# Kernel tuning notes

Measured on AMD Instinct MI355X. Metric: run time of the kernel, lower is better.

Reference implementation:

```python
import jax, jax.numpy as jnp
import numpy as np

IN_SIZE = 256
HID = 256          # memory_vector_size == hidd_size
MEM = 128          # memory_size
ALPHA_SIG = -0.4
GAMMA = 0.3
GATE = 1.0 / (1.0 + np.exp(-ALPHA_SIG))  # sigmoid(alpha_sig) ~ 0.4013
B, T = 128, 1024


def _l2norm(x):
    # F.normalize(x, dim=-1): x / max(||x||2, 1e-12)
    return x / jnp.maximum(jnp.linalg.norm(x, axis=-1, keepdims=True), 1e-12)


def setup_inputs() -> dict:
    key = jax.random.key(0)
    ks = jax.random.split(key, 5)
    s = 1.0 / np.sqrt(HID)  # torch LSTMCell default init range
    X = jax.random.normal(ks[0], (B, T, IN_SIZE), dtype=jnp.float32)
    W_ih = jax.random.uniform(ks[1], (4 * HID, IN_SIZE), jnp.float32, -s, s)
    W_hh = jax.random.uniform(ks[2], (4 * HID, HID), jnp.float32, -s, s)
    b_ih = jax.random.uniform(ks[3], (4 * HID,), jnp.float32, -s, s)
    b_hh = jax.random.uniform(ks[4], (4 * HID,), jnp.float32, -s, s)
    return {"X": X, "W_ih": W_ih, "W_hh": W_hh, "b_ih": b_ih, "b_hh": b_hh}


def _forward(X, W_ih, W_hh, b_ih, b_hh):
    Bt = X.shape[0]
    gate = jnp.asarray(GATE, X.dtype)
    gamma = jnp.asarray(GAMMA, X.dtype)

    def lstm_cell(x, h, c):
        z = x @ W_ih.T + b_ih + h @ W_hh.T + b_hh  # [B, 4H]
        i, f, g, o = jnp.split(z, 4, axis=-1)
        c_new = jax.nn.sigmoid(f) * c + jax.nn.sigmoid(i) * jnp.tanh(g)
        h_new = jax.nn.sigmoid(o) * jnp.tanh(c_new)
        return h_new, c_new

    def step(carry, x_t):
        h, c, M, w_u, prev_w_r = carry
        h, c = lstm_cell(x_t, h, c)
        # read head: softmax over cosine similarity with memory rows
        inner = h @ M.T                                    # [B, MEM]
        denom = (jnp.linalg.norm(h, axis=-1, keepdims=True)
                 * jnp.linalg.norm(M, axis=-1)[None, :])   # [B, MEM]
        w_r = jax.nn.softmax(inner / (denom + 1e-8), axis=-1)
        read = w_r @ M                                     # [B, H]
        out_t = jnp.concatenate([h, read], axis=-1)        # [B, 2H]
        # write (original is under torch.no_grad / detached)
        hs = jax.lax.stop_gradient(h)
        wrs = jax.lax.stop_gradient(w_r)
        w_lu = (1.0 - gate) * jax.nn.one_hot(jnp.argmin(w_u, axis=-1), MEM, dtype=M.dtype)
        w_w = gate * prev_w_r + w_lu                       # [B, MEM]
        M_new = _l2norm(M + w_w.T @ hs)                    # einsum('bi,bj->bij').sum(0) == w_w.T @ h
        w_u_new = _l2norm(gamma * w_u + wrs + w_w)
        return (h, c, M_new, w_u_new, wrs), out_t

    init = (jnp.zeros((Bt, HID), X.dtype),
            jnp.zeros((Bt, HID), X.dtype),
            jnp.zeros((MEM, HID), X.dtype),   # self.M starts as zeros
            jnp.zeros((Bt, MEM), X.dtype),    # w_u
            jnp.zeros((Bt, MEM), X.dtype))    # prev_w_r
    _, ys = jax.lax.scan(step, init, jnp.swapaxes(X, 0, 1))  # ys: [T, B, 2H]
    return jnp.swapaxes(ys, 0, 1)                            # [B, T, 2H]


def reference(X, W_ih, W_hh, b_ih, b_hh):
    return _forward(X, W_ih, W_hh, b_ih, b_hh)
```

## Files before the change

### kernel.cpp

```cpp
#include <hip/hip_runtime.h>
#include <math.h>

#define BATCH 128
#define TSTEPS 1024
#define INSZ 256
#define HSZ 256
#define MEMN 128

#define NWG_A 128
#define NWG_B 64
#define NWG_C 32
#define NWG 224
#define NTHR 256

#define GATE_C 0.40131233988754794f
#define OMG_C  (1.0f - GATE_C)
#define GAMMA_C 0.3f

__device__ float g_hT[(size_t)TSTEPS * HSZ * BATCH];
__device__ float g_M [(size_t)TSTEPS * MEMN * HSZ];
__device__ float g_Mn[(size_t)TSTEPS * MEMN];
__device__ float g_ww[(size_t)TSTEPS * BATCH * MEMN];
__device__ float g_c[BATCH * HSZ];
__device__ int g_fA[TSTEPS * NWG_A];
__device__ int g_fB[TSTEPS * NWG_B];
__device__ int g_fC[TSTEPS * NWG_C];

__global__ void reset_ctrl_kernel() {
    const int gt = blockIdx.x * 256 + threadIdx.x, gn = gridDim.x * 256;
    for (int i = gt; i < TSTEPS * NWG_A; i += gn)
        __hip_atomic_store(&g_fA[i], 0, __ATOMIC_RELAXED, __HIP_MEMORY_SCOPE_AGENT);
    for (int i = gt; i < TSTEPS * NWG_B; i += gn)
        __hip_atomic_store(&g_fB[i], 0, __ATOMIC_RELAXED, __HIP_MEMORY_SCOPE_AGENT);
    for (int i = gt; i < TSTEPS * NWG_C; i += gn)
        __hip_atomic_store(&g_fC[i], 0, __ATOMIC_RELAXED, __HIP_MEMORY_SCOPE_AGENT);
}

__device__ __forceinline__ float sigf(float x) { return 1.0f / (1.0f + expf(-x)); }

__device__ __forceinline__ void st_wt(float* p, float v) {
    __hip_atomic_store(p, v, __ATOMIC_RELAXED, __HIP_MEMORY_SCOPE_AGENT);
}
__device__ __forceinline__ void st_flag(int* p, int v) {
    __hip_atomic_store(p, v, __ATOMIC_RELAXED, __HIP_MEMORY_SCOPE_AGENT);
}
__device__ __forceinline__ void wait_vm0() { asm volatile("s_waitcnt vmcnt(0)" ::: "memory"); }

__device__ __forceinline__ void wait_flags(int* f, int n, int want, int lane) {
    int it = 0;
    for (;;) {
        bool ok = true;
        for (int i = lane; i < n; i += 64)
            ok &= (__hip_atomic_load(&f[i], __ATOMIC_RELAXED, __HIP_MEMORY_SCOPE_AGENT) == want);
        if (__all(ok)) break;
        __builtin_amdgcn_s_sleep(1);
        if (++it > (1 << 22)) break;
    }
}

__global__ void __launch_bounds__(NTHR, 1)
mann_persist(const float* __restrict__ X, const float* __restrict__ Wih,
             const float* __restrict__ Whh, const float* __restrict__ bih,
             const float* __restrict__ bhh, float* __restrict__ out) {
    __shared__ float4 s_x4[64 * 128];
    __shared__ float s_aux[4096];
    __shared__ float s_red8[8];
    __shared__ float s_red16[16];
    __shared__ unsigned long long s_redu8[8];

    const int w = blockIdx.x, tid = threadIdx.x;
    const int lane = tid & 63, wv = tid >> 6;

    auto grpsum = [&](float v) -> float {
#pragma unroll
        for (int o = 32; o; o >>= 1) v += __shfl_xor(v, o, 64);
        if (lane == 0) s_red8[wv] = v;
        __syncthreads();
        float r = s_red8[(tid >> 7) * 2] + s_red8[(tid >> 7) * 2 + 1];
        __syncthreads();
        return r;
    };
    auto grpmax = [&](float v) -> float {
#pragma unroll
        for (int o = 32; o; o >>= 1) v = fmaxf(v, __shfl_xor(v, o, 64));
        if (lane == 0) s_red8[wv] = v;
        __syncthreads();
        float r = fmaxf(s_red8[(tid >> 7) * 2], s_red8[(tid >> 7) * 2 + 1]);
        __syncthreads();
        return r;
    };
    auto grpminu = [&](unsigned long long v) -> unsigned long long {
#pragma unroll
        for (int o = 32; o; o >>= 1) {
            unsigned long long o2 = __shfl_xor(v, o, 64);
            v = (o2 < v) ? o2 : v;
        }
        if (lane == 0) s_redu8[wv] = v;
        __syncthreads();
        unsigned long long a = s_redu8[(tid >> 7) * 2], b2 = s_redu8[(tid >> 7) * 2 + 1];
        unsigned long long r = (a < b2) ? a : b2;
        __syncthreads();
        return r;
    };
    auto red256sum4 = [&](float v0, float v1, float v2, float v3, float (&r)[4]) {
#pragma unroll
        for (int o = 32; o; o >>= 1) {
            v0 += __shfl_xor(v0, o, 64);
            v1 += __shfl_xor(v1, o, 64);
            v2 += __shfl_xor(v2, o, 64);
            v3 += __shfl_xor(v3, o, 64);
        }
        if (lane == 0) {
            s_red16[wv * 4 + 0] = v0; s_red16[wv * 4 + 1] = v1;
            s_red16[wv * 4 + 2] = v2; s_red16[wv * 4 + 3] = v3;
        }
        __syncthreads();
#pragma unroll
        for (int k = 0; k < 4; ++k)
            r[k] = (s_red16[0 * 4 + k] + s_red16[1 * 4 + k]) +
                   (s_red16[2 * 4 + k] + s_red16[3 * 4 + k]);
        __syncthreads();
    };

    if (w < NWG_A) {
        const int bb = w >> 6, jb = w & 63;
        const int bglob = bb * 64 + lane;
        float biasA[4];
#pragma unroll
        for (int g = 0; g < 4; ++g) {
            const int row = g * HSZ + jb * 4 + wv;
            biasA[g] = bih[row] + bhh[row];
        }

        auto stageX = [&](int t) {
            const int kq = tid & 63, bofs = tid >> 6;
#pragma unroll 4
            for (int rep = 0; rep < 16; ++rep) {
                const int b = rep * 4 + bofs;
                const float4 v = *(const float4*)(X + ((size_t)(bb * 64 + b) * TSTEPS + t) * INSZ + kq * 4);
                s_x4[b * 128 + (kq ^ (b & 7))] = v;
            }
        };
        auto computeRegion = [&](float (&acc)[16], const float* __restrict__ Wb, const int kofs) {
            const int kbase = kofs + wv * 64;
#pragma unroll 4
            for (int k4 = 0; k4 < 16; ++k4) {
                const int kg = kbase + k4 * 4;
                const float4 xv = s_x4[lane * 128 + ((kg >> 2) ^ (lane & 7))];
                const int kl = kg - kofs;
#pragma unroll
                for (int rr = 0; rr < 16; ++rr) {
                    const int grow = (rr >> 2) * HSZ + jb * 4 + (rr & 3);
                    const float4 wv4 = *(const float4*)(Wb + (size_t)grow * 256 + kl);
                    acc[rr] += wv4.x * xv.x + wv4.y * xv.y + wv4.z * xv.z + wv4.w * xv.w;
                }
            }
        };

        stageX(0);
        __syncthreads();

        for (int t = 0; t < TSTEPS; ++t) {
            float acc[16];
#pragma unroll
            for (int i = 0; i < 16; ++i) acc[i] = 0.f;
            float4 hv[16];
            if (t > 0) {
                if (wv == 0) wait_flags(g_fA + (size_t)(t - 1) * NWG_A, NWG_A, t, lane);
                __syncthreads();
                asm volatile("" ::: "memory");
#pragma unroll
                for (int rep = 0; rep < 16; ++rep) {
                    const int j0 = (wv * 16 + rep) * 4;
                    const size_t base = ((size_t)(t - 1) * HSZ + j0) * BATCH + bglob;
                    float4 v;
                    v.x = g_hT[base];
                    v.y = g_hT[base + BATCH];
                    v.z = g_hT[base + 2 * BATCH];
                    v.w = g_hT[base + 3 * BATCH];
                    hv[rep] = v;
                }
            }
            computeRegion(acc, Wih, 0);
            if (t > 0) {
#pragma unroll
                for (int rep = 0; rep < 16; ++rep)
                    s_x4[lane * 128 + ((64 + wv * 16 + rep) ^ (lane & 7))] = hv[rep];
            } else {
                const float4 z4 = make_float4(0.f, 0.f, 0.f, 0.f);
#pragma unroll
                for (int rep = 0; rep < 16; ++rep)
                    s_x4[lane * 128 + ((64 + wv * 16 + rep) ^ (lane & 7))] = z4;
            }
            __syncthreads();
            computeRegion(acc, Whh, 256);
#pragma unroll
            for (int rr = 0; rr < 16; ++rr) s_aux[(wv * 16 + rr) * 64 + lane] = acc[rr];
            __syncthreads();
            float z[4];
#pragma unroll
            for (int g = 0; g < 4; ++g) {
                const int rr = g * 4 + wv;
                z[g] = ((s_aux[rr * 64 + lane] + s_aux[(16 + rr) * 64 + lane]) +
                        (s_aux[(32 + rr) * 64 + lane] + s_aux[(48 + rr) * 64 + lane])) + biasA[g];
            }
            const int jglob = jb * 4 + wv;
            const int cidx = bglob * HSZ + jglob;
            const float cold = (t == 0) ? 0.f : g_c[cidx];
            const float cn = sigf(z[1]) * cold + sigf(z[0]) * tanhf(z[2]);
            const float hn = sigf(z[3]) * tanhf(cn);
            g_c[cidx] = cn;
            st_wt(&g_hT[((size_t)t * HSZ + jglob) * BATCH + bglob], hn);
            wait_vm0();
            __syncthreads();
            if (tid == 0) st_flag(&g_fA[(size_t)t * NWG_A + w], t + 1);
            if (t + 1 < TSTEPS) stageX(t + 1);
        }
    } else if (w < NWG_A + NWG_B) {
        const int bwg = w - NWG_A;
        const int grp = tid >> 7, lm = tid & 127;
        const int bB = bwg * 2 + grp;
        float* s_M = (float*)s_x4;
        float* s_h2 = s_aux;
        float* s_wr2 = s_aux + 512;
        float wwreg = (lm == 0) ? OMG_C : 0.f;
        float wureg = 0.f;

        for (int t = 0; t < TSTEPS; ++t) {
            if (t > 0) {
                if (wv == 1) wait_flags(g_fC + (size_t)(t - 1) * NWG_C, NWG_C, t, lane);
                __syncthreads();
                asm volatile("" ::: "memory");
                float4 mt[32];
                const float4* msrc = (const float4*)&g_M[(size_t)t * MEMN * HSZ];
#pragma unroll
                for (int i = 0; i < 32; ++i) mt[i] = msrc[i * 256 + tid];
                float4* md = (float4*)s_M;
#pragma unroll
                for (int i = 0; i < 32; ++i) md[i * 256 + tid] = mt[i];
            }
            if (wv == 0) wait_flags(g_fA + (size_t)t * NWG_A, NWG_A, t + 1, lane);
            __syncthreads();
            asm volatile("" ::: "memory");
            s_h2[grp * 256 + lm] = g_hT[((size_t)t * HSZ + lm) * BATCH + bB];
            s_h2[grp * 256 + lm + 128] = g_hT[((size_t)t * HSZ + lm + 128) * BATCH + bB];
            __syncthreads();
            const float hv0 = s_h2[grp * 256 + lm], hv1 = s_h2[grp * 256 + lm + 128];
            const float hnorm = sqrtf(grpsum(hv0 * hv0 + hv1 * hv1));
            float sc = 0.f;
            if (t > 0) {
                const float4* mrow = (const float4*)&s_M[(size_t)lm * HSZ];
                const float4* h4 = (const float4*)&s_h2[grp * 256];
                const int sw = lm & 7;
                float a = 0.f;
#pragma unroll 8
                for (int c = 0; c < 64; ++c) {
                    const int ci = c ^ sw;
                    const float4 m4 = mrow[ci], x4 = h4[ci];
                    a += m4.x * x4.x + m4.y * x4.y + m4.z * x4.z + m4.w * x4.w;
                }
                const float mn = g_Mn[(size_t)t * MEMN + lm];
                sc = a / (hnorm * mn + 1e-8f);
            }
            const float mx = grpmax(sc);
            const float ev = expf(sc - mx);
            const float es = grpsum(ev);
            const float wr = ev / es;
            s_wr2[grp * 128 + lm] = wr;
            __syncthreads();
            float rd0 = 0.f, rd1 = 0.f;
            if (t > 0) {
#pragma unroll 8
                for (int m = 0; m < 128; ++m) {
                    const float mv = s_M[m * HSZ + tid];
                    rd0 += s_wr2[m] * mv;
                    rd1 += s_wr2[128 + m] * mv;
                }
            }
            const int b0 = bwg * 2, b1 = b0 + 1;
            float* o0 = out + ((size_t)b0 * TSTEPS + t) * 512;
            float* o1 = out + ((size_t)b1 * TSTEPS + t) * 512;
            o0[tid] = s_h2[tid];
            o1[tid] = s_h2[256 + tid];
            o0[256 + tid] = rd0;
            o1[256 + tid] = rd1;
            const float un = GAMMA_C * wureg + wr + wwreg;
            const float un2 = grpsum(un * un);
            const float us = 1.0f / fmaxf(sqrtf(un2), 1e-12f);
            const float wun = un * us;
            wureg = wun;
            unsigned long long key =
                (((unsigned long long)__float_as_uint(wun)) << 32) | (unsigned)lm;
            const unsigned long long mk = grpminu(key);
            const int amin = (int)(mk & 0xffffffffu);
            const float wwn = GATE_C * wr + ((lm == amin) ? OMG_C : 0.f);
            wwreg = wwn;
            if (t + 1 < TSTEPS)
                st_wt(&g_ww[((size_t)(t + 1) * BATCH + bB) * MEMN + lm], wwn);
            wait_vm0();
            __syncthreads();
            if (tid == 0) st_flag(&g_fB[(size_t)t * NWG_B + bwg], t + 1);
        }
    } else {
        const int cwg = w - NWG_A - NWG_B;
        const int m0 = cwg * 4;
        float* s_wwc = s_aux;
        float mreg[4] = {0.f, 0.f, 0.f, 0.f};

        for (int t = 0; t < TSTEPS - 1; ++t) {
            if (wv == 1 && t > 0) wait_flags(g_fB + (size_t)(t - 1) * NWG_B, NWG_B, t, lane);
            __syncthreads();
            asm volatile("" ::: "memory");
            {
                const int e0 = tid, e1 = tid + 256;
                float v0, v1;
                if (t > 0) {
                    v0 = g_ww[((size_t)t * BATCH + (e0 >> 2)) * MEMN + m0 + (e0 & 3)];
                    v1 = g_ww[((size_t)t * BATCH + (e1 >> 2)) * MEMN + m0 + (e1 & 3)];
                } else {
                    v0 = (m0 + (e0 & 3) == 0) ? OMG_C : 0.f;
                    v1 = (m0 + (e1 & 3) == 0) ? OMG_C : 0.f;
                }
                s_wwc[(e0 & 3) * 128 + (e0 >> 2)] = v0;
                s_wwc[(e1 & 3) * 128 + (e1 >> 2)] = v1;
            }
            if (wv == 0) wait_flags(g_fA + (size_t)t * NWG_A, NWG_A, t + 1, lane);
            __syncthreads();
            asm volatile("" ::: "memory");
            float4 hb[32];
            const float4* ht4 = (const float4*)&g_hT[((size_t)t * HSZ + tid) * BATCH];
#pragma unroll
            for (int q = 0; q < 32; ++q) hb[q] = ht4[q];
            float macc[4];
#pragma unroll
            for (int mi = 0; mi < 4; ++mi) macc[mi] = mreg[mi];
#pragma unroll
            for (int b4 = 0; b4 < 32; ++b4) {
                const float4 hv4 = hb[b4];
#pragma unroll
                for (int mi = 0; mi < 4; ++mi) {
                    const float* wc = &s_wwc[mi * 128 + b4 * 4];
                    macc[mi] += wc[0] * hv4.x + wc[1] * hv4.y + wc[2] * hv4.z + wc[3] * hv4.w;
                }
            }
            float nr[4];
            red256sum4(macc[0] * macc[0], macc[1] * macc[1],
                       macc[2] * macc[2], macc[3] * macc[3], nr);
#pragma unroll
            for (int mi = 0; mi < 4; ++mi) {
                const float nrm = sqrtf(nr[mi]);
                const float scale = 1.0f / fmaxf(nrm, 1e-12f);
                const float vo = macc[mi] * scale;
                mreg[mi] = vo;
                st_wt(&g_M[((size_t)(t + 1) * MEMN + m0 + mi) * HSZ + tid], vo);
                if (tid == 0) st_wt(&g_Mn[(size_t)(t + 1) * MEMN + m0 + mi], nrm * scale);
            }
            wait_vm0();
            __syncthreads();
            if (tid == 0) st_flag(&g_fC[(size_t)t * NWG_C + cwg], t + 1);
        }
    }
}

extern "C" void kernel_launch(void* const* d_in, const int* in_sizes, int n_in,
                              void* d_out, int out_size, void* d_ws, size_t ws_size,
                              hipStream_t stream) {
    const float* X   = (const float*)d_in[0];
    const float* Wih = (const float*)d_in[1];
    const float* Whh = (const float*)d_in[2];
    const float* bih = (const float*)d_in[3];
    const float* bhh = (const float*)d_in[4];
    float* out = (float*)d_out;
    (void)in_sizes; (void)n_in; (void)out_size; (void)d_ws; (void)ws_size;

    hipLaunchKernelGGL(reset_ctrl_kernel, dim3(224), dim3(256), 0, stream);
    hipLaunchKernelGGL(mann_persist, dim3(NWG), dim3(NTHR), 0, stream,
                       X, Wih, Whh, bih, bhh, out);
}
```

Before: 24.68 ms.

## Interleave workgroup roles across grid, prefetch X into registers, keep cell state in registers

Workgroup roles are now assigned by blockIdx modulo 8, which interleaves LSTM, read-head and memory-write groups across the device. The grid grows to 256 and class 7 sits idle. The next timestep's X slice is loaded into registers before the W_ih product and the flag wait, so its global latency overlaps compute. The flag wait is split across the four waves, and the LSTM cell state c stays in a register instead of a round trip through global memory. In exchange, register pressure rises from the 16 prefetched float4 values, and 32 extra idle workgroups are launched.

After: 23.69 ms. 1.04x faster.

```diff
diff --git a/kernel.cpp b/kernel.cpp
--- a/kernel.cpp
+++ b/kernel.cpp
@@ -10,7 +10,7 @@
 #define NWG_A 128
 #define NWG_B 64
 #define NWG_C 32
-#define NWG 224
+#define NWG 256
 #define NTHR 256
 
 #define GATE_C 0.40131233988754794f
@@ -21,7 +21,6 @@
 __device__ float g_M [(size_t)TSTEPS * MEMN * HSZ];
 __device__ float g_Mn[(size_t)TSTEPS * MEMN];
 __device__ float g_ww[(size_t)TSTEPS * BATCH * MEMN];
-__device__ float g_c[BATCH * HSZ];
 __device__ int g_fA[TSTEPS * NWG_A];
 __device__ int g_fB[TSTEPS * NWG_B];
 __device__ int g_fC[TSTEPS * NWG_C];
@@ -70,6 +69,7 @@
 
     const int w = blockIdx.x, tid = threadIdx.x;
     const int lane = tid & 63, wv = tid >> 6;
+    const int cls = w & 7, idx8 = w >> 3;
 
     auto grpsum = [&](float v) -> float {
 #pragma unroll
@@ -122,8 +122,10 @@
         __syncthreads();
     };
 
-    if (w < NWG_A) {
-        const int bb = w >> 6, jb = w & 63;
+    if (cls < 4) {
+        const int aidx = cls * 32 + idx8;
+        const int bb = cls >> 1;
+        const int jb = (cls & 1) * 32 + idx8;
         const int bglob = bb * 64 + lane;
         float biasA[4];
 #pragma unroll
@@ -132,13 +134,20 @@
             biasA[g] = bih[row] + bhh[row];
         }
 
-        auto stageX = [&](int t) {
+        auto loadXreg = [&](int t, float4 (&xr)[16]) {
             const int kq = tid & 63, bofs = tid >> 6;
-#pragma unroll 4
+#pragma unroll
             for (int rep = 0; rep < 16; ++rep) {
                 const int b = rep * 4 + bofs;
-                const float4 v = *(const float4*)(X + ((size_t)(bb * 64 + b) * TSTEPS + t) * INSZ + kq * 4);
-                s_x4[b * 128 + (kq ^ (b & 7))] = v;
+                xr[rep] = *(const float4*)(X + ((size_t)(bb * 64 + b) * TSTEPS + t) * INSZ + kq * 4);
+            }
+        };
+        auto storeXlds = [&](float4 (&xr)[16]) {
+            const int kq = tid & 63, bofs = tid >> 6;
+#pragma unroll
+            for (int rep = 0; rep < 16; ++rep) {
+                const int b = rep * 4 + bofs;
+                s_x4[b * 128 + (kq ^ (b & 7))] = xr[rep];
             }
         };
         auto computeRegion = [&](float (&acc)[16], const float* __restrict__ Wb, const int kofs) {
@@ -157,18 +166,27 @@
             }
         };
 
-        stageX(0);
-        __syncthreads();
+        {
+            float4 xr[16];
+            loadXreg(0, xr);
+            storeXlds(xr);
+        }
+        __syncthreads();
+        float creg = 0.f;
 
         for (int t = 0; t < TSTEPS; ++t) {
             float acc[16];
 #pragma unroll
             for (int i = 0; i < 16; ++i) acc[i] = 0.f;
-            float4 hv[16];
+            const bool pf = (t + 1 < TSTEPS);
+            float4 xr[16];
+            if (pf) loadXreg(t + 1, xr);
+            computeRegion(acc, Wih, 0);
             if (t > 0) {
-                if (wv == 0) wait_flags(g_fA + (size_t)(t - 1) * NWG_A, NWG_A, t, lane);
+                wait_flags(g_fA + (size_t)(t - 1) * NWG_A + wv * 32, 32, t, lane);
                 __syncthreads();
                 asm volatile("" ::: "memory");
+                float4 hv[16];
 #pragma unroll
                 for (int rep = 0; rep < 16; ++rep) {
                     const int j0 = (wv * 16 + rep) * 4;
@@ -180,13 +198,13 @@
                     v.w = g_hT[base + 3 * BATCH];
                     hv[rep] = v;
                 }
-            }
-            computeRegion(acc, Wih, 0);
-            if (t > 0) {
+                if (pf) storeXlds(xr);
 #pragma unroll
                 for (int rep = 0; rep < 16; ++rep)
                     s_x4[lane * 128 + ((64 + wv * 16 + rep) ^ (lane & 7))] = hv[rep];
             } else {
+                __syncthreads();
+                if (pf) storeXlds(xr);
                 const float4 z4 = make_float4(0.f, 0.f, 0.f, 0.f);
 #pragma unroll
                 for (int rep = 0; rep < 16; ++rep)
@@ -205,19 +223,16 @@
                         (s_aux[(32 + rr) * 64 + lane] + s_aux[(48 + rr) * 64 + lane])) + biasA[g];
             }
             const int jglob = jb * 4 + wv;
-            const int cidx = bglob * HSZ + jglob;
-            const float cold = (t == 0) ? 0.f : g_c[cidx];
-            const float cn = sigf(z[1]) * cold + sigf(z[0]) * tanhf(z[2]);
+            const float cn = sigf(z[1]) * creg + sigf(z[0]) * tanhf(z[2]);
             const float hn = sigf(z[3]) * tanhf(cn);
-            g_c[cidx] = cn;
+            creg = cn;
             st_wt(&g_hT[((size_t)t * HSZ + jglob) * BATCH + bglob], hn);
             wait_vm0();
             __syncthreads();
-            if (tid == 0) st_flag(&g_fA[(size_t)t * NWG_A + w], t + 1);
-            if (t + 1 < TSTEPS) stageX(t + 1);
-        }
-    } else if (w < NWG_A + NWG_B) {
-        const int bwg = w - NWG_A;
+            if (tid == 0) st_flag(&g_fA[(size_t)t * NWG_A + aidx], t + 1);
+        }
+    } else if (cls < 6) {
+        const int bwg = (cls - 4) * 32 + idx8;
         const int grp = tid >> 7, lm = tid & 127;
         const int bB = bwg * 2 + grp;
         float* s_M = (float*)s_x4;
@@ -301,8 +316,8 @@
             __syncthreads();
             if (tid == 0) st_flag(&g_fB[(size_t)t * NWG_B + bwg], t + 1);
         }
-    } else {
-        const int cwg = w - NWG_A - NWG_B;
+    } else if (cls == 6) {
+        const int cwg = idx8;
         const int m0 = cwg * 4;
         float* s_wwc = s_aux;
         float mreg[4] = {0.f, 0.f, 0.f, 0.f};
```

## Replace persistent flag-synchronised kernel with per-timestep kernel launches

Applied to the files above, without the earlier changes.

Replaces the single persistent kernel, which coordinated LSTM, read-head and memory-write workgroups through spin-waited global flags, with one launch per timestep. Kernel boundaries now provide ordering, and the read/write stages are skewed one step behind the LSTM stage. Recurrent state such as w_u and w_w that used to stay in registers now goes through global memory. The change removes flag polling and cross-workgroup spinning but adds about a thousand launches and their overheads. It also loses the previous overlap of X staging with the wait for the next step.

Measured after the change: 24.56 ms. No clear change (-0.5%).

```diff
diff --git a/kernel.cpp b/kernel.cpp
--- a/kernel.cpp
+++ b/kernel.cpp
@@ -17,51 +17,20 @@
 #define OMG_C  (1.0f - GATE_C)
 #define GAMMA_C 0.3f
 
-__device__ float g_hT[(size_t)TSTEPS * HSZ * BATCH];
-__device__ float g_M [(size_t)TSTEPS * MEMN * HSZ];
-__device__ float g_Mn[(size_t)TSTEPS * MEMN];
-__device__ float g_ww[(size_t)TSTEPS * BATCH * MEMN];
-__device__ float g_c[BATCH * HSZ];
-__device__ int g_fA[TSTEPS * NWG_A];
-__device__ int g_fB[TSTEPS * NWG_B];
-__device__ int g_fC[TSTEPS * NWG_C];
-
-__global__ void reset_ctrl_kernel() {
-    const int gt = blockIdx.x * 256 + threadIdx.x, gn = gridDim.x * 256;
-    for (int i = gt; i < TSTEPS * NWG_A; i += gn)
-        __hip_atomic_store(&g_fA[i], 0, __ATOMIC_RELAXED, __HIP_MEMORY_SCOPE_AGENT);
-    for (int i = gt; i < TSTEPS * NWG_B; i += gn)
-        __hip_atomic_store(&g_fB[i], 0, __ATOMIC_RELAXED, __HIP_MEMORY_SCOPE_AGENT);
-    for (int i = gt; i < TSTEPS * NWG_C; i += gn)
-        __hip_atomic_store(&g_fC[i], 0, __ATOMIC_RELAXED, __HIP_MEMORY_SCOPE_AGENT);
-}
+__device__ float g_hT [(size_t)TSTEPS * HSZ * BATCH];
+__device__ float g_M  [(size_t)TSTEPS * MEMN * HSZ];
+__device__ float g_Mn [(size_t)TSTEPS * MEMN];
+__device__ float g_ww [(size_t)(TSTEPS + 1) * BATCH * MEMN];
+__device__ float g_wu [(size_t)(TSTEPS + 1) * BATCH * MEMN];
+__device__ float g_cst[BATCH * HSZ];
 
 __device__ __forceinline__ float sigf(float x) { return 1.0f / (1.0f + expf(-x)); }
 
-__device__ __forceinline__ void st_wt(float* p, float v) {
-    __hip_atomic_store(p, v, __ATOMIC_RELAXED, __HIP_MEMORY_SCOPE_AGENT);
-}
-__device__ __forceinline__ void st_flag(int* p, int v) {
-    __hip_atomic_store(p, v, __ATOMIC_RELAXED, __HIP_MEMORY_SCOPE_AGENT);
-}
-__device__ __forceinline__ void wait_vm0() { asm volatile("s_waitcnt vmcnt(0)" ::: "memory"); }
-
-__device__ __forceinline__ void wait_flags(int* f, int n, int want, int lane) {
-    int it = 0;
-    for (;;) {
-        bool ok = true;
-        for (int i = lane; i < n; i += 64)
-            ok &= (__hip_atomic_load(&f[i], __ATOMIC_RELAXED, __HIP_MEMORY_SCOPE_AGENT) == want);
-        if (__all(ok)) break;
-        __builtin_amdgcn_s_sleep(1);
-        if (++it > (1 << 22)) break;
-    }
-}
-
 __global__ void __launch_bounds__(NTHR, 1)
-mann_persist(const float* __restrict__ X, const float* __restrict__ Wih,
-             const float* __restrict__ Whh, const float* __restrict__ bih,
-             const float* __restrict__ bhh, float* __restrict__ out) {
+step_kernel(const int t,
+            const float* __restrict__ X, const float* __restrict__ Wih,
+            const float* __restrict__ Whh, const float* __restrict__ bih,
+            const float* __restrict__ bhh, float* __restrict__ out) {
     __shared__ float4 s_x4[64 * 128];
     __shared__ float s_aux[4096];
     __shared__ float s_red8[8];
@@ -123,16 +92,20 @@
     };
 
     if (w < NWG_A) {
+        if (t >= TSTEPS) return;
         const int bb = w >> 6, jb = w & 63;
         const int bglob = bb * 64 + lane;
+        const int jglob = jb * 4 + wv;
+        const int cidx = bglob * HSZ + jglob;
         float biasA[4];
 #pragma unroll
         for (int g = 0; g < 4; ++g) {
             const int row = g * HSZ + jb * 4 + wv;
             biasA[g] = bih[row] + bhh[row];
         }
-
-        auto stageX = [&](int t) {
+        const float cold = (t == 0) ? 0.f : g_cst[cidx];
+
+        {
             const int kq = tid & 63, bofs = tid >> 6;
 #pragma unroll 4
             for (int rep = 0; rep < 16; ++rep) {
@@ -140,8 +113,31 @@
                 const float4 v = *(const float4*)(X + ((size_t)(bb * 64 + b) * TSTEPS + t) * INSZ + kq * 4);
                 s_x4[b * 128 + (kq ^ (b & 7))] = v;
             }
-        };
-        auto computeRegion = [&](float (&acc)[16], const float* __restrict__ Wb, const int kofs) {
+        }
+        float4 hv[16];
+        if (t > 0) {
+#pragma unroll
+            for (int rep = 0; rep < 16; ++rep) {
+                const int j0 = (wv * 16 + rep) * 4;
+                const size_t base = ((size_t)(t - 1) * HSZ + j0) * BATCH + bglob;
+                float4 v;
+                v.x = g_hT[base];
+                v.y = g_hT[base + BATCH];
+                v.z = g_hT[base + 2 * BATCH];
+                v.w = g_hT[base + 3 * BATCH];
+                hv[rep] = v;
+            }
+        } else {
+            const float4 z4 = make_float4(0.f, 0.f, 0.f, 0.f);
+#pragma unroll
+            for (int rep = 0; rep < 16; ++rep) hv[rep] = z4;
+        }
+        __syncthreads();
+
+        float acc[16];
+#pragma unroll
+        for (int i = 0; i < 16; ++i) acc[i] = 0.f;
+        auto computeRegion = [&](float (&a16)[16], const float* __restrict__ Wb, const int kofs) {
             const int kbase = kofs + wv * 64;
 #pragma unroll 4
             for (int k4 = 0; k4 < 16; ++k4) {
@@ -152,212 +148,152 @@
                 for (int rr = 0; rr < 16; ++rr) {
                     const int grow = (rr >> 2) * HSZ + jb * 4 + (rr & 3);
                     const float4 wv4 = *(const float4*)(Wb + (size_t)grow * 256 + kl);
-                    acc[rr] += wv4.x * xv.x + wv4.y * xv.y + wv4.z * xv.z + wv4.w * xv.w;
+                    a16[rr] += wv4.x * xv.x + wv4.y * xv.y + wv4.z * xv.z + wv4.w * xv.w;
                 }
             }
         };
-
-        stageX(0);
-        __syncthreads();
-
-        for (int t = 0; t < TSTEPS; ++t) {
-            float acc[16];
-#pragma unroll
-            for (int i = 0; i < 16; ++i) acc[i] = 0.f;
-            float4 hv[16];
-            if (t > 0) {
-                if (wv == 0) wait_flags(g_fA + (size_t)(t - 1) * NWG_A, NWG_A, t, lane);
-                __syncthreads();
-                asm volatile("" ::: "memory");
-#pragma unroll
-                for (int rep = 0; rep < 16; ++rep) {
-                    const int j0 = (wv * 16 + rep) * 4;
-                    const size_t base = ((size_t)(t - 1) * HSZ + j0) * BATCH + bglob;
-                    float4 v;
-                    v.x = g_hT[base];
-                    v.y = g_hT[base + BATCH];
-                    v.z = g_hT[base + 2 * BATCH];
-                    v.w = g_hT[base + 3 * BATCH];
-                    hv[rep] = v;
-                }
-            }
-            computeRegion(acc, Wih, 0);
-            if (t > 0) {
-#pragma unroll
-                for (int rep = 0; rep < 16; ++rep)
-                    s_x4[lane * 128 + ((64 + wv * 16 + rep) ^ (lane & 7))] = hv[rep];
-            } else {
-                const float4 z4 = make_float4(0.f, 0.f, 0.f, 0.f);
-#pragma unroll
-                for (int rep = 0; rep < 16; ++rep)
-                    s_x4[lane * 128 + ((64 + wv * 16 + rep) ^ (lane & 7))] = z4;
-            }
-            __syncthreads();
-            computeRegion(acc, Whh, 256);
-#pragma unroll
-            for (int rr = 0; rr < 16; ++rr) s_aux[(wv * 16 + rr) * 64 + lane] = acc[rr];
-            __syncthreads();
-            float z[4];
-#pragma unroll
-            for (int g = 0; g < 4; ++g) {
-                const int rr = g * 4 + wv;
-                z[g] = ((s_aux[rr * 64 + lane] + s_aux[(16 + rr) * 64 + lane]) +
-                        (s_aux[(32 + rr) * 64 + lane] + s_aux[(48 + rr) * 64 + lane])) + biasA[g];
-            }
-            const int jglob = jb * 4 + wv;
-            const int cidx = bglob * HSZ + jglob;
-            const float cold = (t == 0) ? 0.f : g_c[cidx];
-            const float cn = sigf(z[1]) * cold + sigf(z[0]) * tanhf(z[2]);
-            const float hn = sigf(z[3]) * tanhf(cn);
-            g_c[cidx] = cn;
-            st_wt(&g_hT[((size_t)t * HSZ + jglob) * BATCH + bglob], hn);
-            wait_vm0();
-            __syncthreads();
-            if (tid == 0) st_flag(&g_fA[(size_t)t * NWG_A + w], t + 1);
-            if (t + 1 < TSTEPS) stageX(t + 1);
-        }
+        computeRegion(acc, Wih, 0);
+#pragma unroll
+        for (int rep = 0; rep < 16; ++rep)
+            s_x4[lane * 128 + ((64 + wv * 16 + rep) ^ (lane & 7))] = hv[rep];
+        __syncthreads();
+        computeRegion(acc, Whh, 256);
+#pragma unroll
+        for (int rr = 0; rr < 16; ++rr) s_aux[(wv * 16 + rr) * 64 + lane] = acc[rr];
+        __syncthreads();
+        float z[4];
+#pragma unroll
+        for (int g = 0; g < 4; ++g) {
+            const int rr = g * 4 + wv;
+            z[g] = ((s_aux[rr * 64 + lane] + s_aux[(16 + rr) * 64 + lane]) +
+                    (s_aux[(32 + rr) * 64 + lane] + s_aux[(48 + rr) * 64 + lane])) + biasA[g];
+        }
+        const float cn = sigf(z[1]) * cold + sigf(z[0]) * tanhf(z[2]);
+        const float hn = sigf(z[3]) * tanhf(cn);
+        g_cst[cidx] = cn;
+        g_hT[((size_t)t * HSZ + jglob) * BATCH + bglob] = hn;
     } else if (w < NWG_A + NWG_B) {
+        if (t < 1) return;
+        const int s = t - 1;
         const int bwg = w - NWG_A;
         const int grp = tid >> 7, lm = tid & 127;
         const int bB = bwg * 2 + grp;
         float* s_M = (float*)s_x4;
         float* s_h2 = s_aux;
         float* s_wr2 = s_aux + 512;
-        float wwreg = (lm == 0) ? OMG_C : 0.f;
-        float wureg = 0.f;
-
-        for (int t = 0; t < TSTEPS; ++t) {
-            if (t > 0) {
-                if (wv == 1) wait_flags(g_fC + (size_t)(t - 1) * NWG_C, NWG_C, t, lane);
-                __syncthreads();
-                asm volatile("" ::: "memory");
-                float4 mt[32];
-                const float4* msrc = (const float4*)&g_M[(size_t)t * MEMN * HSZ];
-#pragma unroll
-                for (int i = 0; i < 32; ++i) mt[i] = msrc[i * 256 + tid];
-                float4* md = (float4*)s_M;
-#pragma unroll
-                for (int i = 0; i < 32; ++i) md[i * 256 + tid] = mt[i];
-            }
-            if (wv == 0) wait_flags(g_fA + (size_t)t * NWG_A, NWG_A, t + 1, lane);
-            __syncthreads();
-            asm volatile("" ::: "memory");
-            s_h2[grp * 256 + lm] = g_hT[((size_t)t * HSZ + lm) * BATCH + bB];
-            s_h2[grp * 256 + lm + 128] = g_hT[((size_t)t * HSZ + lm + 128) * BATCH + bB];
-            __syncthreads();
-            const float hv0 = s_h2[grp * 256 + lm], hv1 = s_h2[grp * 256 + lm + 128];
-            const float hnorm = sqrtf(grpsum(hv0 * hv0 + hv1 * hv1));
-            float sc = 0.f;
-            if (t > 0) {
-                const float4* mrow = (const float4*)&s_M[(size_t)lm * HSZ];
-                const float4* h4 = (const float4*)&s_h2[grp * 256];
-                const int sw = lm & 7;
-                float a = 0.f;
+
+        if (s > 0) {
+            float4 mt[32];
+            const float4* msrc = (const float4*)&g_M[(size_t)s * MEMN * HSZ];
+#pragma unroll
+            for (int i = 0; i < 32; ++i) mt[i] = msrc[i * 256 + tid];
+            float4* md = (float4*)s_M;
+#pragma unroll
+            for (int i = 0; i < 32; ++i) md[i * 256 + tid] = mt[i];
+        }
+        s_h2[grp * 256 + lm] = g_hT[((size_t)s * HSZ + lm) * BATCH + bB];
+        s_h2[grp * 256 + lm + 128] = g_hT[((size_t)s * HSZ + lm + 128) * BATCH + bB];
+        const float wu_prev = (s > 0) ? g_wu[((size_t)s * BATCH + bB) * MEMN + lm] : 0.f;
+        const float ww_prev = (s > 0) ? g_ww[((size_t)s * BATCH + bB) * MEMN + lm]
+                                      : ((lm == 0) ? OMG_C : 0.f);
+        __syncthreads();
+        const float hv0 = s_h2[grp * 256 + lm], hv1 = s_h2[grp * 256 + lm + 128];
+        const float hnorm = sqrtf(grpsum(hv0 * hv0 + hv1 * hv1));
+        float sc = 0.f;
+        if (s > 0) {
+            const float4* mrow = (const float4*)&s_M[(size_t)lm * HSZ];
+            const float4* h4 = (const float4*)&s_h2[grp * 256];
+            const int sw = lm & 7;
+            float a = 0.f;
 #pragma unroll 8
-                for (int c = 0; c < 64; ++c) {
-                    const int ci = c ^ sw;
-                    const float4 m4 = mrow[ci], x4 = h4[ci];
-                    a += m4.x * x4.x + m4.y * x4.y + m4.z * x4.z + m4.w * x4.w;
-                }
-                const float mn = g_Mn[(size_t)t * MEMN + lm];
-                sc = a / (hnorm * mn + 1e-8f);
-            }
-            const float mx = grpmax(sc);
-            const float ev = expf(sc - mx);
-            const float es = grpsum(ev);
-            const float wr = ev / es;
-            s_wr2[grp * 128 + lm] = wr;
-            __syncthreads();
-            float rd0 = 0.f, rd1 = 0.f;
-            if (t > 0) {
+            for (int c = 0; c < 64; ++c) {
+                const int ci = c ^ sw;
+                const float4 m4 = mrow[ci], x4 = h4[ci];
+                a += m4.x * x4.x + m4.y * x4.y + m4.z * x4.z + m4.w * x4.w;
+            }
+            const float mn = g_Mn[(size_t)s * MEMN + lm];
+            sc = a / (hnorm * mn + 1e-8f);
+        }
+        const float mx = grpmax(sc);
+        const float ev = expf(sc - mx);
+        const float es = grpsum(ev);
+        const float wr = ev / es;
+        s_wr2[grp * 128 + lm] = wr;
+        __syncthreads();
+        float rd0 = 0.f, rd1 = 0.f;
+        if (s > 0) {
 #pragma unroll 8
-                for (int m = 0; m < 128; ++m) {
-                    const float mv = s_M[m * HSZ + tid];
-                    rd0 += s_wr2[m] * mv;
-                    rd1 += s_wr2[128 + m] * mv;
-                }
-            }
-            const int b0 = bwg * 2, b1 = b0 + 1;
-            float* o0 = out + ((size_t)b0 * TSTEPS + t) * 512;
-            float* o1 = out + ((size_t)b1 * TSTEPS + t) * 512;
-            o0[tid] = s_h2[tid];
-            o1[tid] = s_h2[256 + tid];
-            o0[256 + tid] = rd0;
-            o1[256 + tid] = rd1;
-            const float un = GAMMA_C * wureg + wr + wwreg;
-            const float un2 = grpsum(un * un);
-            const float us = 1.0f / fmaxf(sqrtf(un2), 1e-12f);
-            const float wun = un * us;
-            wureg = wun;
-            unsigned long long key =
-                (((unsigned long long)__float_as_uint(wun)) << 32) | (unsigned)lm;
-            const unsigned long long mk = grpminu(key);
-            const int amin = (int)(mk & 0xffffffffu);
-            const float wwn = GATE_C * wr + ((lm == amin) ? OMG_C : 0.f);
-            wwreg = wwn;
-            if (t + 1 < TSTEPS)
-                st_wt(&g_ww[((size_t)(t + 1) * BATCH + bB) * MEMN + lm], wwn);
-            wait_vm0();
-            __syncthreads();
-            if (tid == 0) st_flag(&g_fB[(size_t)t * NWG_B + bwg], t + 1);
-        }
-    } else {
+            for (int m = 0; m < 128; ++m) {
+                const float mv = s_M[m * HSZ + tid];
+                rd0 += s_wr2[m] * mv;
+                rd1 += s_wr2[128 + m] * mv;
+            }
+        }
+        const int b0 = bwg * 2, b1 = b0 + 1;
+        float* o0 = out + ((size_t)b0 * TSTEPS + s) * 512;
+        float* o1 = out + ((size_t)b1 * TSTEPS + s) * 512;
+        o0[tid] = s_h2[tid];
+        o1[tid] = s_h2[256 + tid];
+        o0[256 + tid] = rd0;
+        o1[256 + tid] = rd1;
+        const float un = GAMMA_C * wu_prev + wr + ww_prev;
+        const float un2 = grpsum(un * un);
+        const float us = 1.0f / fmaxf(sqrtf(un2), 1e-12f);
+        const float wun = un * us;
+        g_wu[((size_t)(s + 1) * BATCH + bB) * MEMN + lm] = wun;
+        unsigned long long key =
+            (((unsigned long long)__float_as_uint(wun)) << 32) | (unsigned)lm;
+        const unsigned long long mk = grpminu(key);
+        const int amin = (int)(mk & 0xffffffffu);
+        const float wwn = GATE_C * wr + ((lm == amin) ? OMG_C : 0.f);
+        g_ww[((size_t)(s + 1) * BATCH + bB) * MEMN + lm] = wwn;
+    } else if (w < NWG) {
+        if (t < 1 || t - 1 >= TSTEPS - 1) return;
+        const int s = t - 1;
         const int cwg = w - NWG_A - NWG_B;
         const int m0 = cwg * 4;
         float* s_wwc = s_aux;
-        float mreg[4] = {0.f, 0.f, 0.f, 0.f};
-
-        for (int t = 0; t < TSTEPS - 1; ++t) {
-            if (wv == 1 && t > 0) wait_flags(g_fB + (size_t)(t - 1) * NWG_B, NWG_B, t, lane);
-            __syncthreads();
-            asm volatile("" ::: "memory");
-            {
-                const int e0 = tid, e1 = tid + 256;
-                float v0, v1;
-                if (t > 0) {
-                    v0 = g_ww[((size_t)t * BATCH + (e0 >> 2)) * MEMN + m0 + (e0 & 3)];
-                    v1 = g_ww[((size_t)t * BATCH + (e1 >> 2)) * MEMN + m0 + (e1 & 3)];
-                } else {
-                    v0 = (m0 + (e0 & 3) == 0) ? OMG_C : 0.f;
-                    v1 = (m0 + (e1 & 3) == 0) ? OMG_C : 0.f;
-                }
-                s_wwc[(e0 & 3) * 128 + (e0 >> 2)] = v0;
-                s_wwc[(e1 & 3) * 128 + (e1 >> 2)] = v1;
-            }
-            if (wv == 0) wait_flags(g_fA + (size_t)t * NWG_A, NWG_A, t + 1, lane);
-            __syncthreads();
-            asm volatile("" ::: "memory");
-            float4 hb[32];
-            const float4* ht4 = (const float4*)&g_hT[((size_t)t * HSZ + tid) * BATCH];
-#pragma unroll
-            for (int q = 0; q < 32; ++q) hb[q] = ht4[q];
-            float macc[4];
-#pragma unroll
-            for (int mi = 0; mi < 4; ++mi) macc[mi] = mreg[mi];
-#pragma unroll
-            for (int b4 = 0; b4 < 32; ++b4) {
-                const float4 hv4 = hb[b4];
-#pragma unroll
-                for (int mi = 0; mi < 4; ++mi) {
-                    const float* wc = &s_wwc[mi * 128 + b4 * 4];
-                    macc[mi] += wc[0] * hv4.x + wc[1] * hv4.y + wc[2] * hv4.z + wc[3] * hv4.w;
-                }
-            }
-            float nr[4];
-            red256sum4(macc[0] * macc[0], macc[1] * macc[1],
-                       macc[2] * macc[2], macc[3] * macc[3], nr);
+        {
+            const int e0 = tid, e1 = tid + 256;
+            float v0, v1;
+            if (s > 0) {
+                v0 = g_ww[((size_t)s * BATCH + (e0 >> 2)) * MEMN + m0 + (e0 & 3)];
+                v1 = g_ww[((size_t)s * BATCH + (e1 >> 2)) * MEMN + m0 + (e1 & 3)];
+            } else {
+                v0 = (m0 + (e0 & 3) == 0) ? OMG_C : 0.f;
+                v1 = (m0 + (e1 & 3) == 0) ? OMG_C : 0.f;
+            }
+            s_wwc[(e0 & 3) * 128 + (e0 >> 2)] = v0;
+            s_wwc[(e1 & 3) * 128 + (e1 >> 2)] = v1;
+        }
+        float macc[4];
+#pragma unroll
+        for (int mi = 0; mi < 4; ++mi)
+            macc[mi] = (s > 0) ? g_M[((size_t)s * MEMN + m0 + mi) * HSZ + tid] : 0.f;
+        float4 hb[32];
+        const float4* ht4 = (const float4*)&g_hT[((size_t)s * HSZ + tid) * BATCH];
+#pragma unroll
+        for (int q = 0; q < 32; ++q) hb[q] = ht4[q];
+        __syncthreads();
+#pragma unroll
+        for (int b4 = 0; b4 < 32; ++b4) {
+            const float4 hv4 = hb[b4];
 #pragma unroll
             for (int mi = 0; mi < 4; ++mi) {
-                const float nrm = sqrtf(nr[mi]);
-                const float scale = 1.0f / fmaxf(nrm, 1e-12f);
-                const float vo = macc[mi] * scale;
-                mreg[mi] = vo;
-                st_wt(&g_M[((size_t)(t + 1) * MEMN + m0 + mi) * HSZ + tid], vo);
-                if (tid == 0) st_wt(&g_Mn[(size_t)(t + 1) * MEMN + m0 + mi], nrm * scale);
-            }
-            wait_vm0();
-            __syncthreads();
-            if (tid == 0) st_flag(&g_fC[(size_t)t * NWG_C + cwg], t + 1);
+                const float* wc = &s_wwc[mi * 128 + b4 * 4];
+                macc[mi] += wc[0] * hv4.x + wc[1] * hv4.y + wc[2] * hv4.z + wc[3] * hv4.w;
+            }
+        }
+        float nr[4];
+        red256sum4(macc[0] * macc[0], macc[1] * macc[1],
+                   macc[2] * macc[2], macc[3] * macc[3], nr);
+#pragma unroll
+        for (int mi = 0; mi < 4; ++mi) {
+            const float nrm = sqrtf(nr[mi]);
+            const float scale = 1.0f / fmaxf(nrm, 1e-12f);
+            const float vo = macc[mi] * scale;
+            g_M[((size_t)(s + 1) * MEMN + m0 + mi) * HSZ + tid] = vo;
+            if (tid == 0) g_Mn[(size_t)(s + 1) * MEMN + m0 + mi] = nrm * scale;
         }
     }
 }
@@ -373,7 +309,8 @@
     float* out = (float*)d_out;
     (void)in_sizes; (void)n_in; (void)out_size; (void)d_ws; (void)ws_size;
 
-    hipLaunchKernelGGL(reset_ctrl_kernel, dim3(224), dim3(256), 0, stream);
-    hipLaunchKernelGGL(mann_persist, dim3(NWG), dim3(NTHR), 0, stream,
-                       X, Wih, Whh, bih, bhh, out);
+    for (int t = 0; t <= TSTEPS; ++t) {
+        hipLaunchKernelGGL(step_kernel, dim3(NWG), dim3(NTHR), 0, stream,
+                           t, X, Wih, Whh, bih, bhh, out);
+    }
 }
```

## Hoist input projection into parallel pre-kernel and restructure persistent LSTM/memory roles

Applied to the files above, without the earlier changes.

Moves the X·W_ih^T plus bias projection for all timesteps into a separate fully parallel pre-kernel, so the recurrent workgroups only compute h·W_hh^T. The persistent grid becomes 512 blocks with class-interleaved roles that read M straight from global memory instead of staging it in LDS. It also adds batch-major h copies and a local flag chain for LSTM-to-LSTM dependencies. The goal is to shorten the serial per-step critical path, at the cost of a large global z buffer, extra h copies, and reliance on all 512 blocks being co-resident at two per CU.

Measured after the change: 45.33 ms. 83.6% more time.

```diff
diff --git a/kernel.cpp b/kernel.cpp
--- a/kernel.cpp
+++ b/kernel.cpp
@@ -7,37 +7,35 @@
 #define HSZ 256
 #define MEMN 128
 
-#define NWG_A 128
+#define NWG_A 64
 #define NWG_B 64
 #define NWG_C 32
-#define NWG 224
 #define NTHR 256
 
 #define GATE_C 0.40131233988754794f
 #define OMG_C  (1.0f - GATE_C)
 #define GAMMA_C 0.3f
 
+__device__ float g_zx[(size_t)TSTEPS * 4 * HSZ * BATCH];
+__device__ float g_hL[(size_t)TSTEPS * BATCH * HSZ];
+__device__ float g_hB[(size_t)TSTEPS * BATCH * HSZ];
 __device__ float g_hT[(size_t)TSTEPS * HSZ * BATCH];
 __device__ float g_M [(size_t)TSTEPS * MEMN * HSZ];
 __device__ float g_Mn[(size_t)TSTEPS * MEMN];
 __device__ float g_ww[(size_t)TSTEPS * BATCH * MEMN];
-__device__ float g_c[BATCH * HSZ];
-__device__ int g_fA[TSTEPS * NWG_A];
-__device__ int g_fB[TSTEPS * NWG_B];
-__device__ int g_fC[TSTEPS * NWG_C];
+__device__ int g_fAL[TSTEPS * NWG_A];
+__device__ int g_fA [TSTEPS * NWG_A];
+__device__ int g_fB [TSTEPS * NWG_B];
+__device__ int g_fC [TSTEPS * NWG_C];
 
 __global__ void reset_ctrl_kernel() {
     const int gt = blockIdx.x * 256 + threadIdx.x, gn = gridDim.x * 256;
-    for (int i = gt; i < TSTEPS * NWG_A; i += gn)
-        __hip_atomic_store(&g_fA[i], 0, __ATOMIC_RELAXED, __HIP_MEMORY_SCOPE_AGENT);
-    for (int i = gt; i < TSTEPS * NWG_B; i += gn)
-        __hip_atomic_store(&g_fB[i], 0, __ATOMIC_RELAXED, __HIP_MEMORY_SCOPE_AGENT);
-    for (int i = gt; i < TSTEPS * NWG_C; i += gn)
-        __hip_atomic_store(&g_fC[i], 0, __ATOMIC_RELAXED, __HIP_MEMORY_SCOPE_AGENT);
+    for (int i = gt; i < TSTEPS * NWG_A; i += gn) { g_fAL[i] = 0; g_fA[i] = 0; }
+    for (int i = gt; i < TSTEPS * NWG_B; i += gn) g_fB[i] = 0;
+    for (int i = gt; i < TSTEPS * NWG_C; i += gn) g_fC[i] = 0;
 }
 
 __device__ __forceinline__ float sigf(float x) { return 1.0f / (1.0f + expf(-x)); }
-
 __device__ __forceinline__ void st_wt(float* p, float v) {
     __hip_atomic_store(p, v, __ATOMIC_RELAXED, __HIP_MEMORY_SCOPE_AGENT);
 }
@@ -57,19 +55,76 @@
         if (++it > (1 << 22)) break;
     }
 }
-
-__global__ void __launch_bounds__(NTHR, 1)
-mann_persist(const float* __restrict__ X, const float* __restrict__ Wih,
-             const float* __restrict__ Whh, const float* __restrict__ bih,
-             const float* __restrict__ bhh, float* __restrict__ out) {
-    __shared__ float4 s_x4[64 * 128];
-    __shared__ float s_aux[4096];
+__device__ __forceinline__ void wait_local(int* f, int want, int lane) {
+    volatile int* vf = (volatile int*)f;
+    int it = 0;
+    for (;;) {
+        int v = vf[lane];
+        if ((it & 255) == 255)
+            v = __hip_atomic_load(&f[lane], __ATOMIC_RELAXED, __HIP_MEMORY_SCOPE_AGENT);
+        if (__all(v == want)) break;
+        __builtin_amdgcn_s_sleep(1);
+        if (++it > (1 << 22)) break;
+    }
+}
+
+__global__ void __launch_bounds__(NTHR, 2)
+pre_kernel(const float* __restrict__ X, const float* __restrict__ Wih,
+           const float* __restrict__ bih, const float* __restrict__ bhh) {
+    __shared__ float4 p_x[4096];
+    const int w = blockIdx.x, tid = threadIdx.x;
+    const int t = w >> 1, half = w & 1;
+#pragma unroll
+    for (int rep = 0; rep < 16; ++rep) {
+        const int idx = rep * 256 + tid;
+        const int bl = idx >> 6, c = idx & 63;
+        p_x[bl * 64 + (c ^ bl)] =
+            *(const float4*)&X[((size_t)(half * 64 + bl) * TSTEPS + t) * INSZ + c * 4];
+    }
+    __syncthreads();
+    const int bl = tid & 63, hf2 = tid >> 6;
+    const int b = half * 64 + bl;
+    const float4* wih4 = (const float4*)Wih;
+    for (int jb4 = 0; jb4 < 16; ++jb4) {
+        float a16[16];
+#pragma unroll
+        for (int i = 0; i < 16; ++i) a16[i] = 0.f;
+#pragma unroll 4
+        for (int c = 0; c < 64; ++c) {
+            const float4 xv = p_x[bl * 64 + (c ^ bl)];
+#pragma unroll
+            for (int g = 0; g < 4; ++g)
+#pragma unroll
+                for (int j4 = 0; j4 < 4; ++j4) {
+                    const int row = g * HSZ + hf2 * 64 + jb4 * 4 + j4;
+                    const float4 wv4 = wih4[(size_t)row * 64 + c];
+                    a16[g * 4 + j4] += wv4.x * xv.x + wv4.y * xv.y + wv4.z * xv.z + wv4.w * xv.w;
+                }
+        }
+#pragma unroll
+        for (int g = 0; g < 4; ++g)
+#pragma unroll
+            for (int j4 = 0; j4 < 4; ++j4) {
+                const int j = hf2 * 64 + jb4 * 4 + j4;
+                const int row = g * HSZ + j;
+                g_zx[(((size_t)t * 4 + g) * HSZ + j) * BATCH + b] =
+                    a16[g * 4 + j4] + bih[row] + bhh[row];
+            }
+    }
+}
+
+__global__ void __launch_bounds__(NTHR, 2)
+mann_persist(const float* __restrict__ Whh, float* __restrict__ out) {
+    __shared__ float4 s_h4[4096];
+    __shared__ float s_aux[1024];
+    __shared__ float s_tr[512];
     __shared__ float s_red8[8];
     __shared__ float s_red16[16];
     __shared__ unsigned long long s_redu8[8];
 
     const int w = blockIdx.x, tid = threadIdx.x;
     const int lane = tid & 63, wv = tid >> 6;
+    const int cls = w & 7, slot = w >> 3;
 
     auto grpsum = [&](float v) -> float {
 #pragma unroll
@@ -122,141 +177,119 @@
         __syncthreads();
     };
 
-    if (w < NWG_A) {
-        const int bb = w >> 6, jb = w & 63;
-        const int bglob = bb * 64 + lane;
-        float biasA[4];
-#pragma unroll
-        for (int g = 0; g < 4; ++g) {
-            const int row = g * HSZ + jb * 4 + wv;
-            biasA[g] = bih[row] + bhh[row];
-        }
-
-        auto stageX = [&](int t) {
-            const int kq = tid & 63, bofs = tid >> 6;
-#pragma unroll 4
-            for (int rep = 0; rep < 16; ++rep) {
-                const int b = rep * 4 + bofs;
-                const float4 v = *(const float4*)(X + ((size_t)(bb * 64 + b) * TSTEPS + t) * INSZ + kq * 4);
-                s_x4[b * 128 + (kq ^ (b & 7))] = v;
-            }
-        };
-        auto computeRegion = [&](float (&acc)[16], const float* __restrict__ Wb, const int kofs) {
-            const int kbase = kofs + wv * 64;
-#pragma unroll 4
-            for (int k4 = 0; k4 < 16; ++k4) {
-                const int kg = kbase + k4 * 4;
-                const float4 xv = s_x4[lane * 128 + ((kg >> 2) ^ (lane & 7))];
-                const int kl = kg - kofs;
-#pragma unroll
-                for (int rr = 0; rr < 16; ++rr) {
-                    const int grow = (rr >> 2) * HSZ + jb * 4 + (rr & 3);
-                    const float4 wv4 = *(const float4*)(Wb + (size_t)grow * 256 + kl);
-                    acc[rr] += wv4.x * xv.x + wv4.y * xv.y + wv4.z * xv.z + wv4.w * xv.w;
-                }
-            }
-        };
-
-        stageX(0);
-        __syncthreads();
+    if (cls == 0) {
+        const int jblk = slot >> 1, bhalf = slot & 1;
+        const int J = jblk * 8;
+        const int g2 = wv;
+        const int bglob = bhalf * 64 + lane;
+        const float4* wh4 = (const float4*)Whh;
+        float creg[2] = {0.f, 0.f};
 
         for (int t = 0; t < TSTEPS; ++t) {
-            float acc[16];
-#pragma unroll
-            for (int i = 0; i < 16; ++i) acc[i] = 0.f;
-            float4 hv[16];
+            float zr[2][4];
+#pragma unroll
+            for (int jj = 0; jj < 2; ++jj) {
+                const int j = J + g2 * 2 + jj;
+#pragma unroll
+                for (int g = 0; g < 4; ++g)
+                    zr[jj][g] = g_zx[(((size_t)t * 4 + g) * HSZ + j) * BATCH + bglob];
+            }
             if (t > 0) {
-                if (wv == 0) wait_flags(g_fA + (size_t)(t - 1) * NWG_A, NWG_A, t, lane);
+                if (wv == 0) wait_local(g_fAL + (size_t)(t - 1) * NWG_A, t, lane);
                 __syncthreads();
                 asm volatile("" ::: "memory");
 #pragma unroll
                 for (int rep = 0; rep < 16; ++rep) {
-                    const int j0 = (wv * 16 + rep) * 4;
-                    const size_t base = ((size_t)(t - 1) * HSZ + j0) * BATCH + bglob;
-                    float4 v;
-                    v.x = g_hT[base];
-                    v.y = g_hT[base + BATCH];
-                    v.z = g_hT[base + 2 * BATCH];
-                    v.w = g_hT[base + 3 * BATCH];
-                    hv[rep] = v;
-                }
-            }
-            computeRegion(acc, Wih, 0);
+                    const int idx = rep * 256 + tid;
+                    const int bl = idx >> 6, c = idx & 63;
+                    const float4 v = *(const float4*)
+                        &g_hL[((size_t)(t - 1) * BATCH + bhalf * 64 + bl) * HSZ + c * 4];
+                    s_h4[bl * 64 + (c ^ bl)] = v;
+                }
+                __syncthreads();
+            }
+            float acc[2][4] = {{0.f, 0.f, 0.f, 0.f}, {0.f, 0.f, 0.f, 0.f}};
             if (t > 0) {
-#pragma unroll
-                for (int rep = 0; rep < 16; ++rep)
-                    s_x4[lane * 128 + ((64 + wv * 16 + rep) ^ (lane & 7))] = hv[rep];
-            } else {
-                const float4 z4 = make_float4(0.f, 0.f, 0.f, 0.f);
-#pragma unroll
-                for (int rep = 0; rep < 16; ++rep)
-                    s_x4[lane * 128 + ((64 + wv * 16 + rep) ^ (lane & 7))] = z4;
-            }
-            __syncthreads();
-            computeRegion(acc, Whh, 256);
-#pragma unroll
-            for (int rr = 0; rr < 16; ++rr) s_aux[(wv * 16 + rr) * 64 + lane] = acc[rr];
-            __syncthreads();
-            float z[4];
-#pragma unroll
-            for (int g = 0; g < 4; ++g) {
-                const int rr = g * 4 + wv;
-                z[g] = ((s_aux[rr * 64 + lane] + s_aux[(16 + rr) * 64 + lane]) +
-                        (s_aux[(32 + rr) * 64 + lane] + s_aux[(48 + rr) * 64 + lane])) + biasA[g];
-            }
-            const int jglob = jb * 4 + wv;
-            const int cidx = bglob * HSZ + jglob;
-            const float cold = (t == 0) ? 0.f : g_c[cidx];
-            const float cn = sigf(z[1]) * cold + sigf(z[0]) * tanhf(z[2]);
-            const float hn = sigf(z[3]) * tanhf(cn);
-            g_c[cidx] = cn;
-            st_wt(&g_hT[((size_t)t * HSZ + jglob) * BATCH + bglob], hn);
+                const int r0 = J + g2 * 2;
+#pragma unroll 8
+                for (int c = 0; c < 64; ++c) {
+                    const float4 xv = s_h4[lane * 64 + (c ^ lane)];
+#pragma unroll
+                    for (int jj = 0; jj < 2; ++jj)
+#pragma unroll
+                        for (int g = 0; g < 4; ++g) {
+                            const float4 wv4 = wh4[(size_t)(g * HSZ + r0 + jj) * 64 + c];
+                            acc[jj][g] += wv4.x * xv.x + wv4.y * xv.y + wv4.z * xv.z + wv4.w * xv.w;
+                        }
+                }
+            }
+#pragma unroll
+            for (int jj = 0; jj < 2; ++jj) {
+                const float z0 = zr[jj][0] + acc[jj][0];
+                const float z1 = zr[jj][1] + acc[jj][1];
+                const float z2 = zr[jj][2] + acc[jj][2];
+                const float z3 = zr[jj][3] + acc[jj][3];
+                const float cn = sigf(z1) * creg[jj] + sigf(z0) * tanhf(z2);
+                const float hn = sigf(z3) * tanhf(cn);
+                creg[jj] = cn;
+                s_tr[(g2 * 2 + jj) * 64 + lane] = hn;
+            }
+            __syncthreads();
+            if (tid < 64) {
+                const int b = bhalf * 64 + tid;
+                float4 lo, hi;
+                lo.x = s_tr[0 * 64 + tid]; lo.y = s_tr[1 * 64 + tid];
+                lo.z = s_tr[2 * 64 + tid]; lo.w = s_tr[3 * 64 + tid];
+                hi.x = s_tr[4 * 64 + tid]; hi.y = s_tr[5 * 64 + tid];
+                hi.z = s_tr[6 * 64 + tid]; hi.w = s_tr[7 * 64 + tid];
+                *(float4*)&g_hL[((size_t)t * BATCH + b) * HSZ + J] = lo;
+                *(float4*)&g_hL[((size_t)t * BATCH + b) * HSZ + J + 4] = hi;
+            }
             wait_vm0();
             __syncthreads();
-            if (tid == 0) st_flag(&g_fA[(size_t)t * NWG_A + w], t + 1);
-            if (t + 1 < TSTEPS) stageX(t + 1);
-        }
-    } else if (w < NWG_A + NWG_B) {
-        const int bwg = w - NWG_A;
+            if (tid == 0) {
+                *(volatile int*)&g_fAL[(size_t)t * NWG_A + slot] = t + 1;
+                if (t > 0) st_flag(&g_fA[(size_t)(t - 1) * NWG_A + slot], t);
+            }
+            if (tid < 64) {
+                const int b = bhalf * 64 + tid;
+#pragma unroll
+                for (int jj = 0; jj < 8; ++jj) {
+                    const float hv = s_tr[jj * 64 + tid];
+                    st_wt(&g_hB[((size_t)t * BATCH + b) * HSZ + J + jj], hv);
+                    st_wt(&g_hT[((size_t)t * HSZ + J + jj) * BATCH + b], hv);
+                }
+            }
+        }
+        wait_vm0();
+        if (tid == 0) st_flag(&g_fA[(size_t)(TSTEPS - 1) * NWG_A + slot], TSTEPS);
+    } else if (cls == 1) {
+        const int bwg = slot;
         const int grp = tid >> 7, lm = tid & 127;
         const int bB = bwg * 2 + grp;
-        float* s_M = (float*)s_x4;
         float* s_h2 = s_aux;
         float* s_wr2 = s_aux + 512;
         float wwreg = (lm == 0) ? OMG_C : 0.f;
         float wureg = 0.f;
 
         for (int t = 0; t < TSTEPS; ++t) {
-            if (t > 0) {
-                if (wv == 1) wait_flags(g_fC + (size_t)(t - 1) * NWG_C, NWG_C, t, lane);
-                __syncthreads();
-                asm volatile("" ::: "memory");
-                float4 mt[32];
-                const float4* msrc = (const float4*)&g_M[(size_t)t * MEMN * HSZ];
-#pragma unroll
-                for (int i = 0; i < 32; ++i) mt[i] = msrc[i * 256 + tid];
-                float4* md = (float4*)s_M;
-#pragma unroll
-                for (int i = 0; i < 32; ++i) md[i * 256 + tid] = mt[i];
-            }
             if (wv == 0) wait_flags(g_fA + (size_t)t * NWG_A, NWG_A, t + 1, lane);
+            else if (wv == 1 && t > 0) wait_flags(g_fC + (size_t)(t - 1) * NWG_C, NWG_C, t, lane);
             __syncthreads();
             asm volatile("" ::: "memory");
-            s_h2[grp * 256 + lm] = g_hT[((size_t)t * HSZ + lm) * BATCH + bB];
-            s_h2[grp * 256 + lm + 128] = g_hT[((size_t)t * HSZ + lm + 128) * BATCH + bB];
+            s_h2[grp * 256 + lm] = g_hB[((size_t)t * BATCH + bB) * HSZ + lm];
+            s_h2[grp * 256 + lm + 128] = g_hB[((size_t)t * BATCH + bB) * HSZ + 128 + lm];
             __syncthreads();
             const float hv0 = s_h2[grp * 256 + lm], hv1 = s_h2[grp * 256 + lm + 128];
             const float hnorm = sqrtf(grpsum(hv0 * hv0 + hv1 * hv1));
             float sc = 0.f;
             if (t > 0) {
-                const float4* mrow = (const float4*)&s_M[(size_t)lm * HSZ];
+                const float4* mrow = (const float4*)&g_M[((size_t)t * MEMN + lm) * HSZ];
                 const float4* h4 = (const float4*)&s_h2[grp * 256];
-                const int sw = lm & 7;
                 float a = 0.f;
 #pragma unroll 8
                 for (int c = 0; c < 64; ++c) {
-                    const int ci = c ^ sw;
-                    const float4 m4 = mrow[ci], x4 = h4[ci];
+                    const float4 m4 = mrow[c], x4 = h4[c];
                     a += m4.x * x4.x + m4.y * x4.y + m4.z * x4.z + m4.w * x4.w;
                 }
                 const float mn = g_Mn[(size_t)t * MEMN + lm];
@@ -272,7 +305,7 @@
             if (t > 0) {
 #pragma unroll 8
                 for (int m = 0; m < 128; ++m) {
-                    const float mv = s_M[m * HSZ + tid];
+                    const float mv = g_M[((size_t)t * MEMN + m) * HSZ + tid];
                     rd0 += s_wr2[m] * mv;
                     rd1 += s_wr2[128 + m] * mv;
                 }
@@ -301,8 +334,8 @@
             __syncthreads();
             if (tid == 0) st_flag(&g_fB[(size_t)t * NWG_B + bwg], t + 1);
         }
-    } else {
-        const int cwg = w - NWG_A - NWG_B;
+    } else if (cls == 3 && slot < NWG_C) {
+        const int cwg = slot;
         const int m0 = cwg * 4;
         float* s_wwc = s_aux;
         float mreg[4] = {0.f, 0.f, 0.f, 0.f};
@@ -373,7 +406,7 @@
     float* out = (float*)d_out;
     (void)in_sizes; (void)n_in; (void)out_size; (void)d_ws; (void)ws_size;
 
-    hipLaunchKernelGGL(reset_ctrl_kernel, dim3(224), dim3(256), 0, stream);
-    hipLaunchKernelGGL(mann_persist, dim3(NWG), dim3(NTHR), 0, stream,
-                       X, Wih, Whh, bih, bhh, out);
-}
+    hipLaunchKernelGGL(reset_ctrl_kernel, dim3(256), dim3(256), 0, stream);
+    hipLaunchKernelGGL(pre_kernel, dim3(2048), dim3(NTHR), 0, stream, X, Wih, bih, bhh);
+    hipLaunchKernelGGL(mann_persist, dim3(512), dim3(NTHR), 0, stream, Whh, out);
+}
```
